# Kernel tuning notes

Hardware: AMD Instinct MI355X
Metric: run time of the kernel (lower is better)

The kernel has to match this reference:

```python
import jax, jax.numpy as jnp
import numpy as np

# Static config matching init_kwargs
COUT, CIN, K = 64, 64, 3
PAD = K // 2  # padding=1


def setup_inputs() -> dict:
    key = jax.random.key(0)
    k1, k2, k3 = jax.random.split(key, 3)
    B, H, W, FH, FW, SC = 2, 256, 256, 16, 16, 128
    hyper_params = COUT * CIN * K * K  # 36864
    x = jax.random.normal(k1, (B, CIN, H, W), jnp.float32)
    s = jax.random.normal(k2, (B, SC, FH, FW), jnp.float32)
    s2w = jax.random.normal(k3, (hyper_params, SC), jnp.float32) * 0.02
    return {"x": x, "s": s, "s2w": s2w}


def reference(x, s, s2w):
    """HyperPatchConv2d forward: per-patch dynamically generated 3x3 conv.

    x:   [b, c, h, w]   input feature map
    s:   [b, sc, fh, fw] hypernetwork signal (one vector per patch)
    s2w: [P, sc]         signal2weights 1x1 conv (P = out*cin*k*k)
    """
    b, c, h, w = x.shape
    fh, fw = s.shape[-2:]
    ph, pw = h // fh, w // fw          # patch size
    kh, kw = ph + 2 * PAD, pw + 2 * PAD  # unfold window (patch + halo)

    # signal2weights: 1x1 conv -> per-patch flattened conv weight
    wflat = jnp.einsum('pc,bcfg->bfgp', s2w, s)            # [b,fh,fw,P]
    Wdyn = wflat.reshape(b, fh, fw, COUT, CIN, K, K)        # per-patch conv kernels

    # reflect-pad then unfold into overlapping (kh,kw) patches, stride (ph,pw)
    xp = jnp.pad(x, ((0, 0), (0, 0), (PAD, PAD), (PAD, PAD)), mode='reflect')
    idx_h = (jnp.arange(fh) * ph)[:, None] + jnp.arange(kh)[None, :]  # [fh,kh]
    idx_w = (jnp.arange(fw) * pw)[:, None] + jnp.arange(kw)[None, :]  # [fw,kw]
    patches = xp[:, :, idx_h][:, :, :, :, idx_w]            # [b,c,fh,kh,fw,kw]

    # extract KxK sliding windows inside each patch (valid conv, stride 1)
    wi = jnp.arange(ph)[:, None] + jnp.arange(K)[None, :]   # [ph,K]
    wj = jnp.arange(pw)[:, None] + jnp.arange(K)[None, :]   # [pw,K]
    win = patches[:, :, :, wi]                              # [b,c,fh,ph,K,fw,kw]
    win = win[:, :, :, :, :, :, wj]                         # [b,c,fh,ph,K,fw,pw,K]
    win = win.transpose(0, 2, 5, 1, 3, 4, 6, 7)             # [b,fh,fw,c,ph,K,pw,K]

    # per-patch dynamic conv
    out = jnp.einsum('bfgocij,bfgcpiqj->bfgopq', Wdyn, win)  # [b,fh,fw,o,ph,pw]

    # fold: non-overlapping reassembly (stride == patch size)
    return out.transpose(0, 3, 1, 4, 2, 5).reshape(b, COUT, h, w)
```

## Files before the change

kernel.cpp:

```cpp
#include <hip/hip_runtime.h>
#include <hip/hip_bf16.h>


#define C_OUT 64
#define C_IN  64
#define P_TOTAL 36864
#define N_PATCH 512
#define WSTR 72
#define GPLANE 1032
#define BPLANE 520
#define CSTR 136

typedef __bf16 bf16x8 __attribute__((ext_vector_type(8)));
typedef float  f32x4  __attribute__((ext_vector_type(4)));

__device__ __forceinline__ unsigned short f2bf(float f) {
  unsigned int u = __float_as_uint(f);
  u += 0x7fffu + ((u >> 16) & 1u);
  return (unsigned short)(u >> 16);
}

__global__ __launch_bounds__(256) void prep_xs(
    const float* __restrict__ x, const float* __restrict__ s,
    unsigned short* __restrict__ xT, unsigned short* __restrict__ sT) {
  __shared__ unsigned short lds[256 * 68];
  const int bb = blockIdx.x >> 8;
  const int row = blockIdx.x & 255;
  const int t = threadIdx.x;
  const float* src = x + ((size_t)bb * 64) * 65536 + row * 256 + t;
  #pragma unroll 8
  for (int ci = 0; ci < 64; ++ci)
    lds[t * 68 + ci] = f2bf(src[(size_t)ci * 65536]);
  __syncthreads();
  unsigned short* dst = xT + ((size_t)(bb * 65536 + row * 256 + t)) * 64;
  #pragma unroll
  for (int k8 = 0; k8 < 8; ++k8) {
    const uint2 u0 = *(const uint2*)&lds[t * 68 + k8 * 8];
    const uint2 u1 = *(const uint2*)&lds[t * 68 + k8 * 8 + 4];
    *(uint4*)(dst + k8 * 8) = make_uint4(u0.x, u0.y, u1.x, u1.y);
  }
  if (blockIdx.x < 2) {
    const int sb = blockIdx.x;
    unsigned short* sd = sT + ((size_t)sb * 256 + t) * 128;
    for (int k = 0; k < 128; k += 2) {
      const float a = s[(size_t)(sb * 128 + k) * 256 + t];
      const float b = s[(size_t)(sb * 128 + k + 1) * 256 + t];
      *(unsigned int*)(sd + k) = (unsigned int)f2bf(a) | ((unsigned int)f2bf(b) << 16);
    }
  }
}

__global__ __launch_bounds__(256) void wgen_kernel(
    const float* __restrict__ s2w,
    const unsigned short* __restrict__ sT,
    unsigned short* __restrict__ wout)
{
  __shared__ unsigned short As[16 * GPLANE];
  __shared__ unsigned short Bs[16 * BPLANE];
  const int tid = threadIdx.x;
  const int m0 = blockIdx.x * 128;
  const int n0 = blockIdx.y * 64;

  const int fragidx = m0 >> 9;
  const int tap = fragidx >> 3;
  const int ksH = (fragidx >> 2) & 1;
  const int mtH = fragidx & 3;

  #pragma unroll
  for (int i = 0; i < 8; ++i) {
    const int chunk = i * 256 + tid;
    const int row = chunk >> 4;
    const int g = chunk & 15;
    const int m = m0 + row;
    const int j = m & 7;
    const int lane6 = (m >> 3) & 63;
    const int co = mtH * 16 + (lane6 & 15);
    const int ci = ksH * 32 + (lane6 >> 4) * 8 + j;
    const int p = co * 576 + ci * 9 + tap;
    const float* srcp = s2w + (size_t)p * 128 + g * 8;
    const float4 v0 = *(const float4*)srcp;
    const float4 v1 = *(const float4*)(srcp + 4);
    uint4 o;
    o.x = (unsigned int)f2bf(v0.x) | ((unsigned int)f2bf(v0.y) << 16);
    o.y = (unsigned int)f2bf(v0.z) | ((unsigned int)f2bf(v0.w) << 16);
    o.z = (unsigned int)f2bf(v1.x) | ((unsigned int)f2bf(v1.y) << 16);
    o.w = (unsigned int)f2bf(v1.z) | ((unsigned int)f2bf(v1.w) << 16);
    *(uint4*)&As[g * GPLANE + row * 8] = o;
  }
  #pragma unroll
  for (int i = 0; i < 4; ++i) {
    const int chunk = i * 256 + tid;
    const int row = chunk >> 4;
    const int g = chunk & 15;
    *(uint4*)&Bs[g * BPLANE + row * 8] = *(const uint4*)(sT + ((size_t)(n0 + row)) * 128 + g * 8);
  }
  __syncthreads();

  const int wave = tid >> 6;
  const int lane = tid & 63;
  const int col = lane & 15;
  const int quad = lane >> 4;

  f32x4 acc[2][4] = {};
  #pragma unroll
  for (int ks = 0; ks < 4; ++ks) {
    const int g = ks * 4 + quad;
    bf16x8 afr[2], bfr[4];
    #pragma unroll
    for (int mti = 0; mti < 2; ++mti)
      afr[mti] = *(const bf16x8*)&As[g * GPLANE + ((wave * 2 + mti) * 16 + col) * 8];
    #pragma unroll
    for (int nt = 0; nt < 4; ++nt)
      bfr[nt] = *(const bf16x8*)&Bs[g * BPLANE + (nt * 16 + col) * 8];
    #pragma unroll
    for (int mti = 0; mti < 2; ++mti)
      #pragma unroll
      for (int nt = 0; nt < 4; ++nt)
        acc[mti][nt] = __builtin_amdgcn_mfma_f32_16x16x32_bf16(afr[mti], bfr[nt], acc[mti][nt], 0, 0, 0);
  }
  __syncthreads();

  unsigned short* Ct = As;
  #pragma unroll
  for (int mti = 0; mti < 2; ++mti) {
    const int mloc = (wave * 2 + mti) * 16 + quad * 4;
    #pragma unroll
    for (int nt = 0; nt < 4; ++nt) {
      const int pl = nt * 16 + col;
      ushort4 o;
      o.x = f2bf(acc[mti][nt][0]); o.y = f2bf(acc[mti][nt][1]);
      o.z = f2bf(acc[mti][nt][2]); o.w = f2bf(acc[mti][nt][3]);
      *(ushort4*)&Ct[pl * CSTR + mloc] = o;
    }
  }
  __syncthreads();
  #pragma unroll
  for (int i = 0; i < 4; ++i) {
    const int chunk = i * 256 + tid;
    const int pl = chunk >> 4;
    const int ii = chunk & 15;
    const uint4 v = *(const uint4*)&Ct[pl * CSTR + ii * 8];
    *(uint4*)(wout + (size_t)(n0 + pl) * P_TOTAL + m0 + ii * 8) = v;
  }
}

__global__ __launch_bounds__(512) void conv_kernel(
    const unsigned short* __restrict__ xT,
    const unsigned short* __restrict__ wfrag,
    float* __restrict__ out)
{
  __shared__ unsigned short win[324 * WSTR];
  const int tid = threadIdx.x;
  const int patch = blockIdx.x;
  const int bb = patch >> 8;
  const int fg = patch & 255;
  const int f = fg >> 4, g = fg & 15;
  const int row0 = f * 16, col0 = g * 16;

  for (int chunk = tid; chunk < 2592; chunk += 512) {
    const int cell = chunk >> 3;
    const int j = chunk & 7;
    const int r = cell / 18;
    const int c = cell - r * 18;
    int rr = row0 + r - 1; rr = rr < 0 ? -rr : (rr > 255 ? 510 - rr : rr);
    int cc = col0 + c - 1; cc = cc < 0 ? -cc : (cc > 255 ? 510 - cc : cc);
    *(uint4*)&win[cell * WSTR + j * 8] =
        *(const uint4*)(xT + ((size_t)((bb << 16) + (rr << 8) + cc)) * 64 + j * 8);
  }
  __syncthreads();

  const int wave = tid >> 6;
  const int lane = tid & 63;
  const int t = lane & 15;
  const int quad = lane >> 4;
  const int mh = wave & 1;
  const int rq = wave >> 1;

  f32x4 acc[2][4] = {};
  const bf16x8* wb = (const bf16x8*)(wfrag + (size_t)patch * P_TOTAL);

  #pragma unroll
  for (int tap = 0; tap < 9; ++tap) {
    const int ti = tap / 3;
    const int tj = tap - ti * 3;
    bf16x8 afr[2][2];
    #pragma unroll
    for (int ks = 0; ks < 2; ++ks)
      #pragma unroll
      for (int ml = 0; ml < 2; ++ml)
        afr[ks][ml] = wb[((tap * 2 + ks) * 4 + mh * 2 + ml) * 64 + lane];

    #pragma unroll
    for (int nt = 0; nt < 4; ++nt) {
      const int r = rq * 4 + nt + ti;
      const int c = t + tj;
      const int base = (r * 18 + c) * WSTR + quad * 8;
      #pragma unroll
      for (int ks = 0; ks < 2; ++ks) {
        const bf16x8 bfr = *(const bf16x8*)&win[base + ks * 32];
        acc[0][nt] = __builtin_amdgcn_mfma_f32_16x16x32_bf16(afr[ks][0], bfr, acc[0][nt], 0, 0, 0);
        acc[1][nt] = __builtin_amdgcn_mfma_f32_16x16x32_bf16(afr[ks][1], bfr, acc[1][nt], 0, 0, 0);
      }
    }
  }

  #pragma unroll
  for (int ml = 0; ml < 2; ++ml) {
    #pragma unroll
    for (int nt = 0; nt < 4; ++nt) {
      const int p = row0 + rq * 4 + nt;
      #pragma unroll
      for (int reg = 0; reg < 4; ++reg) {
        const int co = (mh * 2 + ml) * 16 + quad * 4 + reg;
        out[(((size_t)bb * C_OUT + co) << 16) + ((size_t)p << 8) + col0 + t] = acc[ml][nt][reg];
      }
    }
  }
}

extern "C" void kernel_launch(void* const* d_in, const int* in_sizes, int n_in,
                              void* d_out, int out_size, void* d_ws, size_t ws_size,
                              hipStream_t stream) {
  const float* x   = (const float*)d_in[0];
  const float* s   = (const float*)d_in[1];
  const float* s2w = (const float*)d_in[2];
  float* out = (float*)d_out;

  char* ws = (char*)d_ws;
  unsigned short* wbuf = (unsigned short*)(ws);
  unsigned short* sT   = (unsigned short*)(ws + 37748736);
  unsigned short* xT   = (unsigned short*)(ws + 37879808);

  prep_xs<<<512, 256, 0, stream>>>(x, s, xT, sT);
  wgen_kernel<<<dim3(288, 8), 256, 0, stream>>>(s2w, sT, wbuf);
  conv_kernel<<<N_PATCH, 512, 0, stream>>>(xT, wbuf, out);
}
```

Before: 133.8 us.

## Pre-pack s2w to bf16 swizzled tiles and load wgen operands via global_load_lds

Merges x/s/s2w preprocessing into one prep kernel that also converts s2w to bf16 once, laid out in XOR-swizzled tile order. The weight-generation GEMM then loads A and B tiles straight into LDS with global_load_lds and widens its N tile from 64 to 128, halving the grid in y. Previously s2w was re-read and re-converted from fp32 by each of the 8 N-blocks; now it is converted once and read 4 times in bf16. The x transpose now uses coalesced float4 loads. The cost is an extra s2w bf16 staging buffer and a round trip through workspace.

```diff
diff --git a/kernel.cpp b/kernel.cpp
--- a/kernel.cpp
+++ b/kernel.cpp
@@ -7,9 +7,7 @@
 #define P_TOTAL 36864
 #define N_PATCH 512
 #define WSTR 72
-#define GPLANE 1032
-#define BPLANE 520
-#define CSTR 136
+#define CSTR2 136
 
 typedef __bf16 bf16x8 __attribute__((ext_vector_type(8)));
 typedef float  f32x4  __attribute__((ext_vector_type(4)));
@@ -19,127 +17,164 @@
   u += 0x7fffu + ((u >> 16) & 1u);
   return (unsigned short)(u >> 16);
 }
-
-__global__ __launch_bounds__(256) void prep_xs(
-    const float* __restrict__ x, const float* __restrict__ s,
-    unsigned short* __restrict__ xT, unsigned short* __restrict__ sT) {
-  __shared__ unsigned short lds[256 * 68];
-  const int bb = blockIdx.x >> 8;
-  const int row = blockIdx.x & 255;
+__device__ __forceinline__ unsigned int pack2(float a, float b) {
+  return (unsigned int)f2bf(a) | ((unsigned int)f2bf(b) << 16);
+}
+__device__ __forceinline__ void gll16(const void* g, void* l) {
+  __builtin_amdgcn_global_load_lds(
+      (const __attribute__((address_space(1))) void*)g,
+      (__attribute__((address_space(3))) void*)l, 16, 0, 0);
+}
+
+__global__ __launch_bounds__(256) void prep_all(
+    const float* __restrict__ x, const float* __restrict__ s, const float* __restrict__ s2w,
+    unsigned short* __restrict__ xT, unsigned short* __restrict__ sTg,
+    unsigned short* __restrict__ s2wP) {
+  __shared__ unsigned short xl[64 * 260];
+  const int bid = blockIdx.x;
   const int t = threadIdx.x;
-  const float* src = x + ((size_t)bb * 64) * 65536 + row * 256 + t;
-  #pragma unroll 8
-  for (int ci = 0; ci < 64; ++ci)
-    lds[t * 68 + ci] = f2bf(src[(size_t)ci * 65536]);
-  __syncthreads();
-  unsigned short* dst = xT + ((size_t)(bb * 65536 + row * 256 + t)) * 64;
-  #pragma unroll
-  for (int k8 = 0; k8 < 8; ++k8) {
-    const uint2 u0 = *(const uint2*)&lds[t * 68 + k8 * 8];
-    const uint2 u1 = *(const uint2*)&lds[t * 68 + k8 * 8 + 4];
-    *(uint4*)(dst + k8 * 8) = make_uint4(u0.x, u0.y, u1.x, u1.y);
-  }
-  if (blockIdx.x < 2) {
-    const int sb = blockIdx.x;
-    unsigned short* sd = sT + ((size_t)sb * 256 + t) * 128;
-    for (int k = 0; k < 128; k += 2) {
-      const float a = s[(size_t)(sb * 128 + k) * 256 + t];
-      const float b = s[(size_t)(sb * 128 + k + 1) * 256 + t];
-      *(unsigned int*)(sd + k) = (unsigned int)f2bf(a) | ((unsigned int)f2bf(b) << 16);
-    }
-  }
-}
-
-__global__ __launch_bounds__(256) void wgen_kernel(
-    const float* __restrict__ s2w,
-    const unsigned short* __restrict__ sT,
-    unsigned short* __restrict__ wout)
-{
-  __shared__ unsigned short As[16 * GPLANE];
-  __shared__ unsigned short Bs[16 * BPLANE];
-  const int tid = threadIdx.x;
-  const int m0 = blockIdx.x * 128;
-  const int n0 = blockIdx.y * 64;
-
-  const int fragidx = m0 >> 9;
+
+  if (bid < 32) {
+    const int sb = bid >> 4;
+    const int g = bid & 15;
+    float v[8];
+    #pragma unroll
+    for (int e = 0; e < 8; ++e)
+      v[e] = s[((size_t)(sb * 128 + g * 8 + e)) * 256 + t];
+    uint4 o;
+    o.x = pack2(v[0], v[1]); o.y = pack2(v[2], v[3]);
+    o.z = pack2(v[4], v[5]); o.w = pack2(v[6], v[7]);
+    const int ntile = sb * 2 + (t >> 7);
+    const int slot = (t & 127) ^ (g & 7);
+    *(uint4*)(sTg + ((size_t)(ntile * 2048 + g * 128 + slot)) * 8) = o;
+    return;
+  }
+
+  if (bid < 544) {
+    const int b2 = bid - 32;
+    const int bb = b2 >> 8, row = b2 & 255;
+    #pragma unroll
+    for (int it = 0; it < 16; ++it) {
+      const int ci = it * 4 + (t >> 6);
+      const int px = (t & 63) * 4;
+      const float4 v = *(const float4*)(x + ((size_t)(bb * 64 + ci)) * 65536 + row * 256 + px);
+      ushort4 o;
+      o.x = f2bf(v.x); o.y = f2bf(v.y); o.z = f2bf(v.z); o.w = f2bf(v.w);
+      *(ushort4*)&xl[ci * 260 + px] = o;
+    }
+    __syncthreads();
+    unsigned short* dst = xT + ((size_t)((bb << 16) + (row << 8) + t)) * 64;
+    #pragma unroll
+    for (int k8 = 0; k8 < 8; ++k8) {
+      const unsigned int w0 = (unsigned int)xl[(k8 * 8 + 0) * 260 + t] |
+                              ((unsigned int)xl[(k8 * 8 + 1) * 260 + t] << 16);
+      const unsigned int w1 = (unsigned int)xl[(k8 * 8 + 2) * 260 + t] |
+                              ((unsigned int)xl[(k8 * 8 + 3) * 260 + t] << 16);
+      const unsigned int w2 = (unsigned int)xl[(k8 * 8 + 4) * 260 + t] |
+                              ((unsigned int)xl[(k8 * 8 + 5) * 260 + t] << 16);
+      const unsigned int w3 = (unsigned int)xl[(k8 * 8 + 6) * 260 + t] |
+                              ((unsigned int)xl[(k8 * 8 + 7) * 260 + t] << 16);
+      *(uint4*)(dst + k8 * 8) = make_uint4(w0, w1, w2, w3);
+    }
+    return;
+  }
+
+  const int b3 = bid - 544;
+  const int m = b3 * 64 + (t >> 2);
+  const int q = t & 3;
+  const int j = m & 7;
+  const int lane6 = (m >> 3) & 63;
+  const int fragidx = m >> 9;
   const int tap = fragidx >> 3;
   const int ksH = (fragidx >> 2) & 1;
   const int mtH = fragidx & 3;
-
-  #pragma unroll
-  for (int i = 0; i < 8; ++i) {
-    const int chunk = i * 256 + tid;
-    const int row = chunk >> 4;
-    const int g = chunk & 15;
-    const int m = m0 + row;
-    const int j = m & 7;
-    const int lane6 = (m >> 3) & 63;
-    const int co = mtH * 16 + (lane6 & 15);
-    const int ci = ksH * 32 + (lane6 >> 4) * 8 + j;
-    const int p = co * 576 + ci * 9 + tap;
-    const float* srcp = s2w + (size_t)p * 128 + g * 8;
-    const float4 v0 = *(const float4*)srcp;
-    const float4 v1 = *(const float4*)(srcp + 4);
+  const int co = mtH * 16 + (lane6 & 15);
+  const int ci = ksH * 32 + (lane6 >> 4) * 8 + j;
+  const int p = co * 576 + ci * 9 + tap;
+  const float* src = s2w + (size_t)p * 128 + q * 32;
+  const int mtile = m >> 7;
+  const int r128 = m & 127;
+  #pragma unroll
+  for (int gg = 0; gg < 4; ++gg) {
+    const int g = q * 4 + gg;
+    const float4 v0 = *(const float4*)(src + gg * 8);
+    const float4 v1 = *(const float4*)(src + gg * 8 + 4);
     uint4 o;
-    o.x = (unsigned int)f2bf(v0.x) | ((unsigned int)f2bf(v0.y) << 16);
-    o.y = (unsigned int)f2bf(v0.z) | ((unsigned int)f2bf(v0.w) << 16);
-    o.z = (unsigned int)f2bf(v1.x) | ((unsigned int)f2bf(v1.y) << 16);
-    o.w = (unsigned int)f2bf(v1.z) | ((unsigned int)f2bf(v1.w) << 16);
-    *(uint4*)&As[g * GPLANE + row * 8] = o;
-  }
-  #pragma unroll
-  for (int i = 0; i < 4; ++i) {
-    const int chunk = i * 256 + tid;
-    const int row = chunk >> 4;
-    const int g = chunk & 15;
-    *(uint4*)&Bs[g * BPLANE + row * 8] = *(const uint4*)(sT + ((size_t)(n0 + row)) * 128 + g * 8);
-  }
-  __syncthreads();
-
-  const int wave = tid >> 6;
+    o.x = pack2(v0.x, v0.y); o.y = pack2(v0.z, v0.w);
+    o.z = pack2(v1.x, v1.y); o.w = pack2(v1.z, v1.w);
+    const int slot = r128 ^ (g & 7);
+    *(uint4*)(s2wP + ((size_t)(mtile * 2048 + g * 128 + slot)) * 8) = o;
+  }
+}
+
+__global__ __launch_bounds__(256) void wgen_kernel(
+    const unsigned short* __restrict__ s2wP,
+    const unsigned short* __restrict__ sTg,
+    unsigned short* __restrict__ wout)
+{
+  __shared__ unsigned short lds[32768];
+  unsigned short* As = lds;
+  unsigned short* Bs = lds + 16384;
+  const int tid = threadIdx.x;
+  const int m0 = blockIdx.x * 128;
+  const int n0 = blockIdx.y * 128;
+
+  const unsigned short* srcA = s2wP + ((size_t)blockIdx.x) * 16384;
+  const unsigned short* srcB = sTg + ((size_t)blockIdx.y) * 16384;
+  #pragma unroll
+  for (int i = 0; i < 8; ++i)
+    gll16(srcA + (size_t)(i * 256 + tid) * 8, As + (i * 256 + tid) * 8);
+  #pragma unroll
+  for (int i = 0; i < 8; ++i)
+    gll16(srcB + (size_t)(i * 256 + tid) * 8, Bs + (i * 256 + tid) * 8);
+  __syncthreads();
+
+  const int w = tid >> 6;
   const int lane = tid & 63;
   const int col = lane & 15;
   const int quad = lane >> 4;
 
-  f32x4 acc[2][4] = {};
+  f32x4 acc[2][8] = {};
   #pragma unroll
   for (int ks = 0; ks < 4; ++ks) {
     const int g = ks * 4 + quad;
-    bf16x8 afr[2], bfr[4];
+    const int gb = g * 1024;
+    const int gx = (g & 7) * 8;
+    bf16x8 afr[2], bfr[8];
     #pragma unroll
     for (int mti = 0; mti < 2; ++mti)
-      afr[mti] = *(const bf16x8*)&As[g * GPLANE + ((wave * 2 + mti) * 16 + col) * 8];
-    #pragma unroll
-    for (int nt = 0; nt < 4; ++nt)
-      bfr[nt] = *(const bf16x8*)&Bs[g * BPLANE + (nt * 16 + col) * 8];
+      afr[mti] = *(const bf16x8*)&As[gb + ((((w * 2 + mti) * 16 + col) * 8) ^ gx)];
+    #pragma unroll
+    for (int nt = 0; nt < 8; ++nt)
+      bfr[nt] = *(const bf16x8*)&Bs[gb + (((nt * 16 + col) * 8) ^ gx)];
     #pragma unroll
     for (int mti = 0; mti < 2; ++mti)
       #pragma unroll
-      for (int nt = 0; nt < 4; ++nt)
+      for (int nt = 0; nt < 8; ++nt)
         acc[mti][nt] = __builtin_amdgcn_mfma_f32_16x16x32_bf16(afr[mti], bfr[nt], acc[mti][nt], 0, 0, 0);
   }
   __syncthreads();
 
-  unsigned short* Ct = As;
+  unsigned short* Ct = lds;
   #pragma unroll
   for (int mti = 0; mti < 2; ++mti) {
-    const int mloc = (wave * 2 + mti) * 16 + quad * 4;
-    #pragma unroll
-    for (int nt = 0; nt < 4; ++nt) {
+    const int mloc = (w * 2 + mti) * 16 + quad * 4;
+    #pragma unroll
+    for (int nt = 0; nt < 8; ++nt) {
       const int pl = nt * 16 + col;
       ushort4 o;
       o.x = f2bf(acc[mti][nt][0]); o.y = f2bf(acc[mti][nt][1]);
       o.z = f2bf(acc[mti][nt][2]); o.w = f2bf(acc[mti][nt][3]);
-      *(ushort4*)&Ct[pl * CSTR + mloc] = o;
-    }
-  }
-  __syncthreads();
-  #pragma unroll
-  for (int i = 0; i < 4; ++i) {
+      *(ushort4*)&Ct[pl * CSTR2 + mloc] = o;
+    }
+  }
+  __syncthreads();
+  #pragma unroll
+  for (int i = 0; i < 8; ++i) {
     const int chunk = i * 256 + tid;
     const int pl = chunk >> 4;
     const int ii = chunk & 15;
-    const uint4 v = *(const uint4*)&Ct[pl * CSTR + ii * 8];
+    const uint4 v = *(const uint4*)&Ct[pl * CSTR2 + ii * 8];
     *(uint4*)(wout + (size_t)(n0 + pl) * P_TOTAL + m0 + ii * 8) = v;
   }
 }
@@ -228,10 +263,11 @@
 
   char* ws = (char*)d_ws;
   unsigned short* wbuf = (unsigned short*)(ws);
-  unsigned short* sT   = (unsigned short*)(ws + 37748736);
+  unsigned short* sTg  = (unsigned short*)(ws + 37748736);
   unsigned short* xT   = (unsigned short*)(ws + 37879808);
-
-  prep_xs<<<512, 256, 0, stream>>>(x, s, xT, sT);
-  wgen_kernel<<<dim3(288, 8), 256, 0, stream>>>(s2w, sT, wbuf);
+  unsigned short* s2wP = (unsigned short*)(ws + 54657024);
+
+  prep_all<<<1120, 256, 0, stream>>>(x, s, s2w, xT, sTg, s2wP);
+  wgen_kernel<<<dim3(288, 4), 256, 0, stream>>>(s2wP, sTg, wbuf);
   conv_kernel<<<N_PATCH, 512, 0, stream>>>(xT, wbuf, out);
 }
```

New measurement: 132.1 us. Within noise of the previous version (-1.3%).
